# Performance work log

Measured on AMD Instinct MI355X. Metric: run time of the kernel, lower is better.

## Reference

```python
import jax, jax.numpy as jnp
import numpy as np

B, H, W, C = 2, 64, 64, 1024
L = H * W
HC, WC = 32, 32
NH, DH = 16, 64
NUM_REMAIN = 1638


def setup_inputs() -> dict:
    key = jax.random.key(0)
    ks = jax.random.split(key, 8)
    s = 1.0 / np.sqrt(C)
    x = jax.random.normal(ks[0], (B, L, C), jnp.float32)
    cached_x = jax.random.normal(ks[1], (B, HC, WC, C), jnp.float32)
    W_qkv = jax.random.normal(ks[2], (3 * C, C), jnp.float32) * s
    q_bias = jnp.zeros((C,), jnp.float32)
    v_bias = jnp.zeros((C,), jnp.float32)
    W_proj = jax.random.normal(ks[3], (C, C), jnp.float32) * s
    b_proj = jnp.zeros((C,), jnp.float32)
    scale_mul_log = jnp.full((1, NH, 1, 1), np.log(4.0), jnp.float32)
    # rope cache as (cos, sin) pairs over the flat token axis, DH//2 freqs
    ang = jax.random.uniform(ks[4], (L, DH // 2), jnp.float32) * (2 * np.pi)
    rope_grid = jnp.stack([jnp.cos(ang), jnp.sin(ang)], axis=0)  # (2, L, DH//2)
    return {"x": x, "cached_x": cached_x, "W_qkv": W_qkv, "q_bias": q_bias,
            "v_bias": v_bias, "W_proj": W_proj, "b_proj": b_proj,
            "scale_mul_log": scale_mul_log, "rope_grid": rope_grid,
            "num_remain": NUM_REMAIN}


def reference(x, cached_x, W_qkv, q_bias, v_bias, W_proj, b_proj,
              scale_mul_log, rope_grid, num_remain):
    Bx, Lx, Cx = x.shape
    # --- FastVAR token merge: MSE-to-spatial-mean selection (adaptive_avg_pool2d -> mean over L)
    mean_x = jnp.mean(x, axis=1, keepdims=True)                      # (B,1,C)
    mse = jnp.sum((x - mean_x) ** 2, axis=-1)                        # (B,L)
    idx = jnp.argsort(-mse, axis=1)[:, :num_remain]                  # (B,n) descending
    bix = jnp.arange(Bx)[:, None]
    xm = x[bix, idx]                                                 # (B,n,C) merged tokens
    # --- qkv projection with (q_bias, 0, v_bias)
    bias = jnp.concatenate([q_bias, jnp.zeros_like(q_bias), v_bias])
    qkv = (xm @ W_qkv.T + bias).reshape(Bx, -1, 3, NH, DH)
    qkv = qkv.transpose(2, 0, 3, 1, 4)                               # (3,B,H,n,dh)
    q, k, v = qkv[0], qkv[1], qkv[2]
    # --- cos attention: L2-normalize q,k; head-wise learned scale on q; sdpa scale = 1
    scale_mul = jnp.exp(jnp.minimum(scale_mul_log, jnp.log(100.0)))  # (1,NH,1,1)
    def l2n(t):
        return t / jnp.maximum(jnp.linalg.norm(t, axis=-1, keepdims=True), 1e-12)
    q = l2n(q) * scale_mul
    k = l2n(k)
    # --- 2D RoPE with per-sample gathered cache at the kept-token positions
    rc = rope_grid[:, idx, :]                                        # (2,B,n,DH//2)
    r0 = rc[0][:, None, :, :]                                        # (B,1,n,DH//2)
    r1 = rc[1][:, None, :, :]
    def rope(t):
        tp = t.reshape(*t.shape[:-1], DH // 2, 2)
        t0, t1 = tp[..., 0], tp[..., 1]
        return jnp.stack([r0 * t0 - r1 * t1, r1 * t0 + r0 * t1], axis=-1).reshape(t.shape)
    q = rope(q)
    k = rope(k)
    # --- attention over merged tokens
    attn = jax.nn.softmax(jnp.einsum('bhqd,bhkd->bhqk', q, k), axis=-1)
    o = jnp.einsum('bhqk,bhkd->bhqd', attn, v)                       # (B,H,n,dh)
    o = o.transpose(0, 2, 1, 3).reshape(Bx, -1, Cx)                  # (B,n,C)
    o = o @ W_proj.T + b_proj
    up = jnp.repeat(jnp.repeat(cached_x, 2, axis=1), 2, axis=2).reshape(Bx, Lx, Cx)
    out_full = up.at[bix, idx].set(o)
    return x + out_full
```

## Files before the change

kernel.cpp:

```cpp
#include <hip/hip_runtime.h>
#include <hip/hip_bf16.h>
#include <math.h>

#define BQ   2
#define LQ   4096
#define CQ   1024
#define NHQ  16
#define DHQ  64
#define KSEL 1638
#define KPAD 1664
#define MTOT (BQ*KSEL)
#define MPAD 3328

typedef short s16x8 __attribute__((ext_vector_type(8)));
typedef float fx4   __attribute__((ext_vector_type(4)));

#define MFMA16(a,b,c) __builtin_amdgcn_mfma_f32_16x16x32_bf16(a,b,c,0,0,0)

__device__ __forceinline__ float b2f(unsigned short u) {
  union { float f; unsigned int i; } cv; cv.i = ((unsigned int)u) << 16; return cv.f;
}
__device__ __forceinline__ unsigned short f2b(float f) {
  union { float f; unsigned int i; } cv; cv.f = f;
  unsigned int x = cv.i;
  return (unsigned short)((x + 0x7fffu + ((x >> 16) & 1u)) >> 16);
}
__device__ __forceinline__ unsigned int fbits(float f) {
  union { float f; unsigned int i; } cv; cv.f = f; return cv.i;
}
__device__ __forceinline__ unsigned int cvtpk_bf16(float a, float b) {
  unsigned int r;
  asm("v_cvt_pk_bf16_f32 %0, %1, %2" : "=v"(r) : "v"(a), "v"(b));
  return r;
}
__device__ __forceinline__ void async16(const void* g, void* l) {
  __builtin_amdgcn_global_load_lds((const __attribute__((address_space(1))) void*)g,
                                   (__attribute__((address_space(3))) void*)l, 16, 0, 0);
}
__device__ __forceinline__ float fexp2(float x) {
#if __has_builtin(__builtin_amdgcn_exp2f)
  return __builtin_amdgcn_exp2f(x);
#else
  return __expf(x * 0.69314718055994531f);
#endif
}

__global__ __launch_bounds__(256) void k_mean_part(const float* __restrict__ x,
                                                   double* __restrict__ part) {
  int bid = blockIdx.x;
  int cb = bid & 3, ch = (bid >> 2) & 31, b = bid >> 7;
  int c = cb * 256 + threadIdx.x;
  const float* p = x + ((size_t)b * LQ + (size_t)ch * 128) * CQ + c;
  double s = 0.0;
  for (int r = 0; r < 128; ++r) s += (double)p[(size_t)r * CQ];
  part[((size_t)b * 32 + ch) * CQ + c] = s;
}

__global__ __launch_bounds__(256) void k_mean_reduce(const double* __restrict__ part,
                                                     double* __restrict__ mean) {
  int g = blockIdx.x * 256 + threadIdx.x;
  int b = g >> 10, c = g & 1023;
  double s = 0.0;
  for (int ch = 0; ch < 32; ++ch) s += part[((size_t)b * 32 + ch) * CQ + c];
  mean[g] = s * (1.0 / 4096.0);
}

__global__ __launch_bounds__(256) void k_mse_base(const float* __restrict__ x,
                                                  const float* __restrict__ cached,
                                                  const double* __restrict__ mean,
                                                  double* __restrict__ mse,
                                                  float* __restrict__ out,
                                                  unsigned short* __restrict__ xb) {
  int bl = blockIdx.x; int b = bl >> 12, l = bl & 4095;
  int hh = l >> 6, ww = l & 63;
  size_t xoff = ((size_t)b * LQ + l) * CQ;
  size_t uoff = (((size_t)b * 32 + (hh >> 1)) * 32 + (ww >> 1)) * CQ;
  const double* mrow = mean + (size_t)b * CQ;
  int c0 = threadIdx.x * 4;
  float4 xv = *(const float4*)(x + xoff + c0);
  float4 uv = *(const float4*)(cached + uoff + c0);
  float4 ov;
  ov.x = xv.x + uv.x; ov.y = xv.y + uv.y; ov.z = xv.z + uv.z; ov.w = xv.w + uv.w;
  *(float4*)(out + xoff + c0) = ov;
  ushort4 xo;
  xo.x = f2b(xv.x); xo.y = f2b(xv.y); xo.z = f2b(xv.z); xo.w = f2b(xv.w);
  ((ushort4*)xb)[(xoff + c0) >> 2] = xo;
  double d0 = (double)xv.x - mrow[c0];
  double d1 = (double)xv.y - mrow[c0 + 1];
  double d2 = (double)xv.z - mrow[c0 + 2];
  double d3 = (double)xv.w - mrow[c0 + 3];
  double ss = d0 * d0 + d1 * d1 + d2 * d2 + d3 * d3;
  for (int o = 1; o < 64; o <<= 1) ss += __shfl_xor(ss, o);
  __shared__ double ws4[4];
  if ((threadIdx.x & 63) == 0) ws4[threadIdx.x >> 6] = ss;
  __syncthreads();
  if (threadIdx.x == 0) mse[(size_t)b * LQ + l] = ws4[0] + ws4[1] + ws4[2] + ws4[3];
}

__global__ __launch_bounds__(1024) void k_topk(const double* __restrict__ mse,
                                               int* __restrict__ idx_sel,
                                               const float* __restrict__ wqkv,
                                               const float* __restrict__ wproj,
                                               unsigned short* __restrict__ wqb,
                                               unsigned short* __restrict__ wpb) {
  if (blockIdx.x >= 2) {
    int i = (blockIdx.x - 2) * 1024 + threadIdx.x;
    const float* s; unsigned short* d; int off;
    if (i < 786432) { s = wqkv;  d = wqb; off = i; }
    else            { s = wproj; d = wpb; off = i - 786432; }
    float4 v = ((const float4*)s)[off];
    ushort4 o;
    o.x = f2b(v.x); o.y = f2b(v.y); o.z = f2b(v.z); o.w = f2b(v.w);
    ((ushort4*)d)[off] = o;
    return;
  }
  __shared__ unsigned long long u[4096];
  __shared__ unsigned int whist[16 * 257];
  __shared__ unsigned int wtot[4];
  __shared__ unsigned long long sh_prefix;
  __shared__ int sh_rem, sh_rem2, sh_bsel, sh_cnt, sh_eqcnt;
  __shared__ int eqbuf[256];
  int b = blockIdx.x, t = threadIdx.x;
  int wv = t >> 6, laneid = t & 63;
  for (int p = 0; p < 4; ++p) {
    int i = p * 1024 + t;
    u[i] = (unsigned long long)__double_as_longlong(mse[(size_t)b * LQ + i]);
  }
  if (t == 0) { sh_prefix = 0ULL; sh_rem = KSEL; sh_cnt = 0; sh_eqcnt = 0; }
  __syncthreads();
  for (int shift = 56; shift >= 0; shift -= 8) {
    for (int z = t; z < 16 * 257; z += 1024) whist[z] = 0u;
    __syncthreads();
    unsigned long long pref = sh_prefix;
#pragma unroll
    for (int p = 0; p < 4; ++p) {
      int i = p * 1024 + t;
      unsigned long long v = u[i];
      bool cand = (shift == 56) || ((v >> ((shift + 8) & 63)) == pref);
      if (cand) atomicAdd(&whist[wv * 257 + ((unsigned int)(v >> shift) & 255u)], 1u);
    }
    __syncthreads();
    unsigned int myc = 0, mysc = 0;
    if (t < 256) {
      unsigned int s = 0;
      int bin = 255 - t;
#pragma unroll
      for (int wvi = 0; wvi < 16; ++wvi) s += whist[wvi * 257 + bin];
      myc = s;
      mysc = myc;
#pragma unroll
      for (int o = 1; o < 64; o <<= 1) {
        unsigned int v2 = __shfl_up(mysc, o);
        if (laneid >= o) mysc += v2;
      }
      if (laneid == 63) wtot[wv] = mysc;
    }
    __syncthreads();
    if (t < 256) {
      unsigned int basep = 0;
      for (int wvi = 0; wvi < wv; ++wvi) basep += wtot[wvi];
      unsigned int incl = basep + mysc;
      unsigned int excl = incl - myc;
      unsigned int rem = (unsigned int)sh_rem;
      if (excl < rem && rem <= incl) {
        sh_bsel = 255 - t;
        sh_rem2 = (int)(rem - excl);
      }
    }
    __syncthreads();
    if (t == 0) {
      sh_prefix = (sh_prefix << 8) | (unsigned long long)sh_bsel;
      sh_rem = sh_rem2;
    }
    __syncthreads();
  }
  unsigned long long T = sh_prefix;
  int rem_eq = sh_rem;
#pragma unroll
  for (int p = 0; p < 4; ++p) {
    int i = p * 1024 + t;
    unsigned long long v = u[i];
    bool win = (v > T);
    unsigned long long mask = __ballot(win);
    int total = __popcll(mask);
    int base = 0;
    if (laneid == 0 && total > 0) base = atomicAdd(&sh_cnt, total);
    base = __shfl(base, 0);
    if (win) {
      int lpos = __popcll(mask & ((1ULL << laneid) - 1ULL));
      idx_sel[b * KPAD + base + lpos] = i;
    }
    if (v == T) {
      int e = atomicAdd(&sh_eqcnt, 1);
      if (e < 256) eqbuf[e] = i;
    }
  }
  __syncthreads();
  if (t == 0) {
    int n = sh_eqcnt; if (n > 256) n = 256;
    for (int a = 1; a < n; ++a) {
      int key = eqbuf[a]; int c = a - 1;
      while (c >= 0 && eqbuf[c] > key) { eqbuf[c + 1] = eqbuf[c]; --c; }
      eqbuf[c + 1] = key;
    }
    int base = sh_cnt;
    for (int a = 0; a < rem_eq && a < n; ++a) idx_sel[b * KPAD + base + a] = eqbuf[a];
    for (int a = KSEL; a < KPAD; ++a) idx_sel[b * KPAD + a] = 0;
  }
}

__global__ __launch_bounds__(256) void k_gemmA(const unsigned short* __restrict__ Asrc,
                                               const unsigned short* __restrict__ Bmat,
                                               const int* __restrict__ idx_sel,
                                               unsigned short* __restrict__ Cbf) {
  int bm = blockIdx.x % 52, bn = blockIdx.x / 52;
  int tid = threadIdx.x;
  int w = tid >> 6, lane = tid & 63, quad = lane >> 4, l15 = lane & 15;
  int wm = w & 1, wn = w >> 1;
  __shared__ __align__(16) unsigned char sm[2][12288];

  const unsigned short* gA;
  {
    int row = tid >> 2, kc = tid & 3;
    int m = bm * 64 + row; if (m >= MTOT) m = MTOT - 1;
    int bb = m / KSEL; int ii = m - bb * KSEL;
    int lsel = idx_sel[bb * KPAD + ii];
    gA = Asrc + ((size_t)bb * LQ + lsel) * CQ + kc * 8;
  }
  const unsigned short* gB[2];
#pragma unroll
  for (int p = 0; p < 2; ++p) {
    int e = p * 256 + tid; int row = e >> 2, kc = e & 3;
    gB[p] = Bmat + (size_t)(bn * 128 + row) * CQ + kc * 8;
  }

  fx4 acc[2][4];
#pragma unroll
  for (int a = 0; a < 2; ++a)
#pragma unroll
    for (int c = 0; c < 4; ++c) acc[a][c] = (fx4){0.f, 0.f, 0.f, 0.f};

#define STAGE_A(buf, it) do { int ke = (it) * 32;                                   \
    async16(gA + ke, sm[buf] + tid * 16);                                           \
    async16(gB[0] + ke, sm[buf] + 4096 + tid * 16);                                 \
    async16(gB[1] + ke, sm[buf] + 8192 + tid * 16); } while (0)

  STAGE_A(0, 0);
  for (int it = 0; it < 32; ++it) {
    int cur = it & 1;
    if (it < 31) STAGE_A(cur ^ 1, it + 1);
    if (it < 31) asm volatile("s_waitcnt vmcnt(3)");
    else         asm volatile("s_waitcnt vmcnt(0)");
    __builtin_amdgcn_s_barrier();
    const unsigned char* smb = sm[cur];
    s16x8 af[2], bf[4];
#pragma unroll
    for (int mt = 0; mt < 2; ++mt)
      af[mt] = *(const s16x8*)(smb + ((wm * 32 + mt * 16 + l15) * 32 + quad * 8) * 2);
#pragma unroll
    for (int nt = 0; nt < 4; ++nt)
      bf[nt] = *(const s16x8*)(smb + 4096 + ((wn * 64 + nt * 16 + l15) * 32 + quad * 8) * 2);
    __builtin_amdgcn_s_setprio(1);
#pragma unroll
    for (int mt = 0; mt < 2; ++mt)
#pragma unroll
      for (int nt = 0; nt < 4; ++nt)
        acc[mt][nt] = MFMA16(af[mt], bf[nt], acc[mt][nt]);
    __builtin_amdgcn_s_setprio(0);
    __builtin_amdgcn_s_barrier();
  }
#undef STAGE_A

#pragma unroll
  for (int mt = 0; mt < 2; ++mt)
#pragma unroll
    for (int nt = 0; nt < 4; ++nt) {
      int n = bn * 128 + wn * 64 + nt * 16 + l15;
      int mbase = bm * 64 + wm * 32 + mt * 16 + quad * 4;
      fx4 vv = acc[mt][nt];
#pragma unroll
      for (int r = 0; r < 4; ++r) {
        int m = mbase + r;
        if (m < MTOT) Cbf[(size_t)m * 3072 + n] = f2b(vv[r]);
      }
    }
}

__global__ __launch_bounds__(256) void k_gemmB(const unsigned short* __restrict__ Asrc,
                                               const unsigned short* __restrict__ Bmat,
                                               const int* __restrict__ idx_sel,
                                               float* __restrict__ Cf,
                                               const float* __restrict__ xin,
                                               const float* __restrict__ bproj) {
  int bid = blockIdx.x;
  int swz = (bid & 7) * 104 + (bid >> 3);
  int bm = swz % 52, bn = swz / 52;
  int tid = threadIdx.x;
  int w = tid >> 6, lane = tid & 63, quad = lane >> 4, l15 = lane & 15;
  int wm = w & 1, wn = w >> 1;
  __shared__ __align__(16) unsigned char sm[2][16384];

  const unsigned short* g4[4];
#pragma unroll
  for (int p = 0; p < 4; ++p) {
    int e = (p & 1) * 256 + tid; int row = e >> 3, kc = e & 7;
    if (p < 2) {
      int m = bm * 64 + row; if (m >= MTOT) m = MTOT - 1;
      int bb = m / KSEL; int ii = m - bb * KSEL;
      g4[p] = Asrc + ((size_t)bb * KPAD + ii) * CQ + kc * 8;
    } else {
      g4[p] = Bmat + (size_t)(bn * 64 + row) * CQ + kc * 8;
    }
  }

  fx4 acc[2][2];
#pragma unroll
  for (int a = 0; a < 2; ++a)
#pragma unroll
    for (int c = 0; c < 2; ++c) acc[a][c] = (fx4){0.f, 0.f, 0.f, 0.f};

#define STAGE_B(buf, it) do { int ke = (it) * 64;                                   \
    _Pragma("unroll")                                                               \
    for (int p = 0; p < 4; ++p)                                                     \
      async16(g4[p] + ke, sm[buf] + p * 4096 + w * 1024);                           \
    } while (0)

  STAGE_B(0, 0);
  for (int it = 0; it < 16; ++it) {
    int cur = it & 1;
    if (it < 15) STAGE_B(cur ^ 1, it + 1);
    if (it < 15) asm volatile("s_waitcnt vmcnt(4)");
    else         asm volatile("s_waitcnt vmcnt(0)");
    __builtin_amdgcn_s_barrier();
    const unsigned char* smb = sm[cur];
#pragma unroll
    for (int kk = 0; kk < 2; ++kk) {
      s16x8 af[2], bf2[2];
#pragma unroll
      for (int mt = 0; mt < 2; ++mt)
        af[mt] = *(const s16x8*)(smb + ((wm * 32 + mt * 16 + l15) * 64 + kk * 32 + quad * 8) * 2);
#pragma unroll
      for (int nt = 0; nt < 2; ++nt)
        bf2[nt] = *(const s16x8*)(smb + 8192 + ((wn * 32 + nt * 16 + l15) * 64 + kk * 32 + quad * 8) * 2);
#pragma unroll
      for (int mt = 0; mt < 2; ++mt)
#pragma unroll
        for (int nt = 0; nt < 2; ++nt)
          acc[mt][nt] = MFMA16(af[mt], bf2[nt], acc[mt][nt]);
    }
    __builtin_amdgcn_s_barrier();
  }
#undef STAGE_B

#pragma unroll
  for (int mt = 0; mt < 2; ++mt)
#pragma unroll
    for (int nt = 0; nt < 2; ++nt) {
      int n = bn * 64 + wn * 32 + nt * 16 + l15;
      int mbase = bm * 64 + wm * 32 + mt * 16 + quad * 4;
      fx4 vv = acc[mt][nt];
      float bp = bproj[n];
#pragma unroll
      for (int r = 0; r < 4; ++r) {
        int m = mbase + r;
        if (m < MTOT) {
          int bb = m / KSEL; int ii = m - bb * KSEL;
          int lsel = idx_sel[bb * KPAD + ii];
          size_t off = ((size_t)bb * LQ + lsel) * CQ + n;
          Cf[off] = xin[off] + vv[r] + bp;
        }
      }
    }
}

__global__ __launch_bounds__(256) void k_normrope(const unsigned short* __restrict__ qkv,
                                                  const int* __restrict__ idx_sel,
                                                  const float* __restrict__ qbias,
                                                  const float* __restrict__ vbias,
                                                  const float* __restrict__ sml,
                                                  const float* __restrict__ rope,
                                                  unsigned short* __restrict__ qo,
                                                  unsigned short* __restrict__ ko,
                                                  unsigned short* __restrict__ vt) {
  int bid = blockIdx.x;
  int tile = bid % 26; int h = (bid / 26) & 15; int b = bid / (26 * 16);
  int tid = threadIdx.x; int w = tid >> 6; int lane = tid & 63;
  int tk = lane >> 5, dl = lane & 31;
  int d0 = dl * 2;
  __shared__ unsigned short vtile[64 * 68];
  float scale = expf(fminf(sml[h], 4.6051702f)) * 1.4426950408889634f;
  float2 qb2 = *(const float2*)(qbias + h * 64 + d0);
  float2 vb2 = *(const float2*)(vbias + h * 64 + d0);
  for (int pass = 0; pass < 8; ++pass) {
    int il = pass * 8 + w * 2 + tk;
    int i = tile * 64 + il;
    float v0 = 0.f, v1 = 0.f;
    if (i < KSEL) {
      int lsel = idx_sel[b * KPAD + i];
      size_t base = ((size_t)(b * KSEL + i)) * 3072 + h * 64 + d0;
      float r0 = rope[(size_t)lsel * 32 + dl];
      float r1 = rope[(size_t)LQ * 32 + (size_t)lsel * 32 + dl];
      unsigned int qw = *(const unsigned int*)(qkv + base);
      float q0 = b2f((unsigned short)qw) + qb2.x;
      float q1 = b2f((unsigned short)(qw >> 16)) + qb2.y;
      float ss = q0 * q0 + q1 * q1;
#pragma unroll
      for (int o = 1; o < 32; o <<= 1) ss += __shfl_xor(ss, o);
      float rn = scale / fmaxf(sqrtf(ss), 1e-12f);
      float qn0 = q0 * rn, qn1 = q1 * rn;
      *(unsigned int*)(qo + ((size_t)(b * NHQ + h) * KPAD + i) * 64 + d0) =
          cvtpk_bf16(r0 * qn0 - r1 * qn1, r1 * qn0 + r0 * qn1);
      unsigned int kw = *(const unsigned int*)(qkv + base + 1024);
      float k0 = b2f((unsigned short)kw);
      float k1 = b2f((unsigned short)(kw >> 16));
      float ks = k0 * k0 + k1 * k1;
#pragma unroll
      for (int o = 1; o < 32; o <<= 1) ks += __shfl_xor(ks, o);
      float rkn = 1.0f / fmaxf(sqrtf(ks), 1e-12f);
      float kn0 = k0 * rkn, kn1 = k1 * rkn;
      *(unsigned int*)(ko + ((size_t)(b * NHQ + h) * KPAD + i) * 64 + d0) =
          cvtpk_bf16(r0 * kn0 - r1 * kn1, r1 * kn0 + r0 * kn1);
      unsigned int vw = *(const unsigned int*)(qkv + base + 2048);
      v0 = b2f((unsigned short)vw) + vb2.x;
      v1 = b2f((unsigned short)(vw >> 16)) + vb2.y;
    }
    vtile[d0 * 68 + il] = f2b(v0);
    vtile[(d0 + 1) * 68 + il] = f2b(v1);
  }
  __syncthreads();
  int row = tid >> 2, c0 = (tid & 3) * 16;
  s16x8 o0, o1;
#pragma unroll
  for (int jj = 0; jj < 8; ++jj) {
    o0[jj] = (short)vtile[row * 68 + c0 + jj];
    o1[jj] = (short)vtile[row * 68 + c0 + 8 + jj];
  }
  size_t doff = ((size_t)((b * NHQ + h) * 64 + row)) * KPAD + (size_t)tile * 64 + c0;
  *(s16x8*)(vt + doff) = o0;
  *(s16x8*)(vt + doff + 8) = o1;
}

__global__ __launch_bounds__(256, 4) void k_attn(const unsigned short* __restrict__ qb,
                                                 const unsigned short* __restrict__ kb,
                                                 const unsigned short* __restrict__ vtb,
                                                 const float* __restrict__ sml,
                                                 unsigned short* __restrict__ pO,
                                                 float* __restrict__ pl) {
  int qt = blockIdx.x; int bh = blockIdx.y; int part = blockIdx.z;
  int b = bh >> 4, h = bh & 15;
  int t0 = part * 13, t1 = t0 + 13;
  int q0 = qt * 128;
  int tid = threadIdx.x, w = tid >> 6, lane = tid & 63, quad = lane >> 4, l15 = lane & 15;
  float M = __expf(fminf(sml[h], 4.6051702f)) * 1.4426950408889634f;
  __shared__ __align__(16) unsigned short Kt[64 * 72];
  __shared__ __align__(16) unsigned short Vt[64 * 72];
  __shared__ __align__(16) unsigned short Pq[4][32 * 72];
  unsigned short* Pw = Pq[w];
  const unsigned short* qbase = qb + (size_t)(b * NHQ + h) * KPAD * 64;
  const unsigned short* kbase = kb + (size_t)(b * NHQ + h) * KPAD * 64;
  const unsigned short* vbase = vtb + (size_t)(b * NHQ + h) * 64 * KPAD;

  int r0 = tid >> 3, c0 = tid & 7;
  int r1 = 32 + r0, c1 = c0;

  s16x8 qf[2][2];
#pragma unroll
  for (int qtile = 0; qtile < 2; ++qtile)
#pragma unroll
    for (int kb2 = 0; kb2 < 2; ++kb2) {
      int row = q0 + w * 32 + qtile * 16 + l15;
      qf[qtile][kb2] = *(const s16x8*)(qbase + (size_t)row * 64 + kb2 * 32 + quad * 8);
    }

  float lsum[2] = {0.f, 0.f};
  fx4 oacc[2][4];
#pragma unroll
  for (int qtile = 0; qtile < 2; ++qtile)
#pragma unroll
    for (int dt = 0; dt < 4; ++dt) oacc[qtile][dt] = (fx4){0.f, 0.f, 0.f, 0.f};

  s16x8 kn0, kn1, vn0, vn1;
  {
    int j0 = t0 * 64;
    kn0 = *(const s16x8*)(kbase + (size_t)(j0 + r0) * 64 + c0 * 8);
    kn1 = *(const s16x8*)(kbase + (size_t)(j0 + r1) * 64 + c1 * 8);
    vn0 = *(const s16x8*)(vbase + (size_t)r0 * KPAD + j0 + c0 * 8);
    vn1 = *(const s16x8*)(vbase + (size_t)r1 * KPAD + j0 + c1 * 8);
  }

  for (int t = t0; t < t1; ++t) {
    int j0 = t * 64;
    bool tail = (j0 + 64 > KSEL);
    __builtin_amdgcn_s_barrier();
    *(s16x8*)(Kt + r0 * 72 + c0 * 8) = kn0;
    *(s16x8*)(Kt + r1 * 72 + c1 * 8) = kn1;
    *(s16x8*)(Vt + r0 * 72 + c0 * 8) = vn0;
    *(s16x8*)(Vt + r1 * 72 + c1 * 8) = vn1;
    if (t + 1 < t1) {
      int jn = (t + 1) * 64;
      kn0 = *(const s16x8*)(kbase + (size_t)(jn + r0) * 64 + c0 * 8);
      kn1 = *(const s16x8*)(kbase + (size_t)(jn + r1) * 64 + c1 * 8);
      vn0 = *(const s16x8*)(vbase + (size_t)r0 * KPAD + jn + c0 * 8);
      vn1 = *(const s16x8*)(vbase + (size_t)r1 * KPAD + jn + c1 * 8);
    }
    asm volatile("s_waitcnt lgkmcnt(0)" ::: "memory");
    __builtin_amdgcn_s_barrier();

    fx4 sacc[2][4];
#pragma unroll
    for (int qtile = 0; qtile < 2; ++qtile)
#pragma unroll
      for (int jj = 0; jj < 4; ++jj) sacc[qtile][jj] = (fx4){0.f, 0.f, 0.f, 0.f};
    __builtin_amdgcn_s_setprio(1);
#pragma unroll
    for (int jj = 0; jj < 4; ++jj) {
      int jl = jj * 16 + l15;
      s16x8 kf0 = *(const s16x8*)(Kt + jl * 72 + quad * 8);
      s16x8 kf1 = *(const s16x8*)(Kt + jl * 72 + 32 + quad * 8);
      sacc[0][jj] = MFMA16(kf0, qf[0][0], sacc[0][jj]);
      sacc[1][jj] = MFMA16(kf0, qf[1][0], sacc[1][jj]);
      sacc[0][jj] = MFMA16(kf1, qf[0][1], sacc[0][jj]);
      sacc[1][jj] = MFMA16(kf1, qf[1][1], sacc[1][jj]);
    }
    __builtin_amdgcn_s_setprio(0);
#pragma unroll
    for (int qtile = 0; qtile < 2; ++qtile)
#pragma unroll
      for (int jj = 0; jj < 4; ++jj) {
        int jbase = j0 + jj * 16 + quad * 4;
        fx4 sv = sacc[qtile][jj];
        float p0 = fexp2(sv[0] - M);
        float p1 = fexp2(sv[1] - M);
        float p2 = fexp2(sv[2] - M);
        float p3 = fexp2(sv[3] - M);
        if (tail) {
          if (jbase + 0 >= KSEL) p0 = 0.f;
          if (jbase + 1 >= KSEL) p1 = 0.f;
          if (jbase + 2 >= KSEL) p2 = 0.f;
          if (jbase + 3 >= KSEL) p3 = 0.f;
        }
        lsum[qtile] += (p0 + p1) + (p2 + p3);
        *(uint2*)(Pw + (qtile * 16 + l15) * 72 + jj * 16 + quad * 4) =
            make_uint2(cvtpk_bf16(p0, p1), cvtpk_bf16(p2, p3));
      }
    __builtin_amdgcn_s_setprio(1);
#pragma unroll
    for (int js = 0; js < 2; ++js) {
      s16x8 pf0 = *(const s16x8*)(Pw + l15 * 72 + js * 32 + quad * 8);
      s16x8 pf1 = *(const s16x8*)(Pw + (16 + l15) * 72 + js * 32 + quad * 8);
#pragma unroll
      for (int dt = 0; dt < 4; ++dt) {
        s16x8 vf = *(const s16x8*)(Vt + (dt * 16 + l15) * 72 + js * 32 + quad * 8);
        oacc[0][dt] = MFMA16(pf0, vf, oacc[0][dt]);
        oacc[1][dt] = MFMA16(pf1, vf, oacc[1][dt]);
      }
    }
    __builtin_amdgcn_s_setprio(0);
  }

#pragma unroll
  for (int qtile = 0; qtile < 2; ++qtile) {
    float s = lsum[qtile];
    s += __shfl_xor(s, 16);
    s += __shfl_xor(s, 32);
    lsum[qtile] = s;
  }

  size_t pbase = (((size_t)part * 2 + b) * NHQ + h) * KPAD;
#pragma unroll
  for (int qtile = 0; qtile < 2; ++qtile) {
    int gqb = q0 + w * 32 + qtile * 16;
    if (quad == 0) pl[pbase + gqb + l15] = lsum[qtile];
  }

#pragma unroll
  for (int qtile = 0; qtile < 2; ++qtile)
#pragma unroll
    for (int dt = 0; dt < 4; ++dt)
#pragma unroll
      for (int r = 0; r < 4; ++r)
        Pw[(qtile * 16 + quad * 4 + r) * 72 + dt * 16 + l15] = f2b(oacc[qtile][dt][r]);
#pragma unroll
  for (int pass = 0; pass < 4; ++pass) {
    int row = pass * 8 + (lane >> 3), chunk = lane & 7;
    s16x8 vv = *(const s16x8*)(Pw + row * 72 + chunk * 8);
    *(s16x8*)(pO + (pbase + q0 + w * 32 + row) * 64 + chunk * 8) = vv;
  }
}

__global__ __launch_bounds__(256) void k_comb(const unsigned short* __restrict__ pO,
                                              const float* __restrict__ pl,
                                              unsigned short* __restrict__ ob) {
  size_t g = (size_t)blockIdx.x * 256 + threadIdx.x;
  int d = (int)(g & 63);
  size_t row = g >> 6;
  int gq = (int)(row % KPAD);
  int bhh = (int)(row / KPAD);
  int b = bhh >> 4, h = bhh & 15;
  float oa = b2f(pO[g]);
  float obv = b2f(pO[g + 3407872]);
  float la = pl[row], lb = pl[row + 53248];
  float o = (oa + obv) / (la + lb);
  ob[((size_t)(b * KPAD + gq)) * CQ + h * 64 + d] = f2b(o);
}

extern "C" void kernel_launch(void* const* d_in, const int* in_sizes, int n_in,
                              void* d_out, int out_size, void* d_ws, size_t ws_size,
                              hipStream_t stream) {
  const float* x      = (const float*)d_in[0];
  const float* cached = (const float*)d_in[1];
  const float* wqkv   = (const float*)d_in[2];
  const float* qbias  = (const float*)d_in[3];
  const float* vbias  = (const float*)d_in[4];
  const float* wproj  = (const float*)d_in[5];
  const float* bproj  = (const float*)d_in[6];
  const float* sml    = (const float*)d_in[7];
  const float* rope   = (const float*)d_in[8];
  float* out = (float*)d_out;
  char* ws = (char*)d_ws;

  double* meanpart        = (double*)(ws);
  double* mean            = (double*)(ws + 524288);
  double* mse             = (double*)(ws + 540672);
  int* idx_sel            = (int*)(ws + 606208);
  unsigned short* x_bf    = (unsigned short*)(ws + 619520);
  unsigned short* wqkv_bf = (unsigned short*)(ws + 17396736);
  unsigned short* qkv     = (unsigned short*)(ws + 23688192);
  unsigned short* pO      = (unsigned short*)(ws + 619520);
  float* pl               = (float*)(ws + 14251008);
  unsigned short* wproj_bf= (unsigned short*)(ws + 44135424);
  unsigned short* qo      = (unsigned short*)(ws + 46232576);
  unsigned short* ko      = (unsigned short*)(ws + 53048320);
  unsigned short* vt      = (unsigned short*)(ws + 59864064);
  unsigned short* ob      = (unsigned short*)(ws + 66679808);

  hipLaunchKernelGGL(k_mean_part, dim3(256), dim3(256), 0, stream, x, meanpart);
  hipLaunchKernelGGL(k_mean_reduce, dim3(8), dim3(256), 0, stream, meanpart, mean);
  hipLaunchKernelGGL(k_mse_base, dim3(8192), dim3(256), 0, stream, x, cached, mean, mse,
                     out, x_bf);
  hipLaunchKernelGGL(k_topk, dim3(2 + 1024), dim3(1024), 0, stream, mse, idx_sel,
                     wqkv, wproj, wqkv_bf, wproj_bf);
  hipLaunchKernelGGL(k_gemmA, dim3(52 * 24), dim3(256), 0, stream,
                     x_bf, wqkv_bf, idx_sel, qkv);
  hipLaunchKernelGGL(k_normrope, dim3(26 * 16 * BQ), dim3(256), 0, stream,
                     qkv, idx_sel, qbias, vbias, sml, rope, qo, ko, vt);
  hipLaunchKernelGGL(k_attn, dim3(13, BQ * NHQ, 2), dim3(256), 0, stream,
                     qo, ko, vt, sml, pO, pl);
  hipLaunchKernelGGL(k_comb, dim3(13312), dim3(256), 0, stream, pO, pl, ob);
  hipLaunchKernelGGL(k_gemmB, dim3(832), dim3(256), 0, stream,
                     ob, wproj_bf, idx_sel, out, x, bproj);
}
```

Before: 279.5 us.

## Split attention KV across three parts, vectorize combine, swizzle QKV GEMM blocks

The attention kernel now splits the key range into three partitions (9/9/8 tiles) instead of two, raising the grid from 832 to 1248 blocks so more CUs are busy. The combine kernel is rewritten to sum three partials and to process 8 elements per thread with 128-bit loads and stores plus a reciprocal multiply. The QKV GEMM block index is swizzled to improve L2 locality between neighbouring blocks. The cost is a larger partial buffer, which is relocated in the workspace, and extra combine traffic.

```diff
diff --git a/kernel.cpp b/kernel.cpp
--- a/kernel.cpp
+++ b/kernel.cpp
@@ -213,7 +213,9 @@
                                                const unsigned short* __restrict__ Bmat,
                                                const int* __restrict__ idx_sel,
                                                unsigned short* __restrict__ Cbf) {
-  int bm = blockIdx.x % 52, bn = blockIdx.x / 52;
+  int bid = blockIdx.x;
+  int swz = (bid & 7) * 156 + (bid >> 3);
+  int bm = swz % 52, bn = swz / 52;
   int tid = threadIdx.x;
   int w = tid >> 6, lane = tid & 63, quad = lane >> 4, l15 = lane & 15;
   int wm = w & 1, wn = w >> 1;
@@ -448,7 +450,8 @@
                                                  float* __restrict__ pl) {
   int qt = blockIdx.x; int bh = blockIdx.y; int part = blockIdx.z;
   int b = bh >> 4, h = bh & 15;
-  int t0 = part * 13, t1 = t0 + 13;
+  int t0 = part * 9;
+  int t1 = (part == 2) ? 26 : t0 + 9;
   int q0 = qt * 128;
   int tid = threadIdx.x, w = tid >> 6, lane = tid & 63, quad = lane >> 4, l15 = lane & 15;
   float M = __expf(fminf(sml[h], 4.6051702f)) * 1.4426950408889634f;
@@ -591,17 +594,32 @@
 __global__ __launch_bounds__(256) void k_comb(const unsigned short* __restrict__ pO,
                                               const float* __restrict__ pl,
                                               unsigned short* __restrict__ ob) {
-  size_t g = (size_t)blockIdx.x * 256 + threadIdx.x;
-  int d = (int)(g & 63);
-  size_t row = g >> 6;
+  size_t g8 = (size_t)blockIdx.x * 256 + threadIdx.x;
+  size_t base = g8 * 8;
+  int d0 = (int)(base & 63);
+  size_t row = base >> 6;
   int gq = (int)(row % KPAD);
   int bhh = (int)(row / KPAD);
   int b = bhh >> 4, h = bhh & 15;
-  float oa = b2f(pO[g]);
-  float obv = b2f(pO[g + 3407872]);
-  float la = pl[row], lb = pl[row + 53248];
-  float o = (oa + obv) / (la + lb);
-  ob[((size_t)(b * KPAD + gq)) * CQ + h * 64 + d] = f2b(o);
+  uint4 p0 = *(const uint4*)(pO + base);
+  uint4 p1 = *(const uint4*)(pO + base + 3407872);
+  uint4 p2 = *(const uint4*)(pO + base + 2 * 3407872);
+  float ls = pl[row] + pl[row + 53248] + pl[row + 2 * 53248];
+  float rc = 1.0f / ls;
+  unsigned int pw0[4] = {p0.x, p0.y, p0.z, p0.w};
+  unsigned int pw1[4] = {p1.x, p1.y, p1.z, p1.w};
+  unsigned int pw2[4] = {p2.x, p2.y, p2.z, p2.w};
+  unsigned int ow[4];
+#pragma unroll
+  for (int j = 0; j < 4; ++j) {
+    float lo = (b2f((unsigned short)pw0[j]) + b2f((unsigned short)pw1[j]) +
+                b2f((unsigned short)pw2[j])) * rc;
+    float hi = (b2f((unsigned short)(pw0[j] >> 16)) + b2f((unsigned short)(pw1[j] >> 16)) +
+                b2f((unsigned short)(pw2[j] >> 16))) * rc;
+    ow[j] = cvtpk_bf16(lo, hi);
+  }
+  *(uint4*)(ob + ((size_t)(b * KPAD + gq)) * CQ + h * 64 + d0) =
+      make_uint4(ow[0], ow[1], ow[2], ow[3]);
 }
 
 extern "C" void kernel_launch(void* const* d_in, const int* in_sizes, int n_in,
@@ -627,7 +645,7 @@
   unsigned short* wqkv_bf = (unsigned short*)(ws + 17396736);
   unsigned short* qkv     = (unsigned short*)(ws + 23688192);
   unsigned short* pO      = (unsigned short*)(ws + 619520);
-  float* pl               = (float*)(ws + 14251008);
+  float* pl               = (float*)(ws + 21066752);
   unsigned short* wproj_bf= (unsigned short*)(ws + 44135424);
   unsigned short* qo      = (unsigned short*)(ws + 46232576);
   unsigned short* ko      = (unsigned short*)(ws + 53048320);
@@ -644,9 +662,9 @@
                      x_bf, wqkv_bf, idx_sel, qkv);
   hipLaunchKernelGGL(k_normrope, dim3(26 * 16 * BQ), dim3(256), 0, stream,
                      qkv, idx_sel, qbias, vbias, sml, rope, qo, ko, vt);
-  hipLaunchKernelGGL(k_attn, dim3(13, BQ * NHQ, 2), dim3(256), 0, stream,
+  hipLaunchKernelGGL(k_attn, dim3(13, BQ * NHQ, 3), dim3(256), 0, stream,
                      qo, ko, vt, sml, pO, pl);
-  hipLaunchKernelGGL(k_comb, dim3(13312), dim3(256), 0, stream, pO, pl, ob);
+  hipLaunchKernelGGL(k_comb, dim3(1664), dim3(256), 0, stream, pO, pl, ob);
   hipLaunchKernelGGL(k_gemmB, dim3(832), dim3(256), 0, stream,
                      ob, wproj_bf, idx_sel, out, x, bproj);
 }
```

Result: no change. 277.2 us (-0.8%).
